# Optimization experiments

Hardware: AMD Instinct MI355X
Metric: run time of the kernel (lower is better)

The kernel has to match this reference:

```python
import jax, jax.numpy as jnp
import numpy as np

KS = (8, 8, 8)   # kernel_size
ST = (4, 4, 4)   # stride


def setup_inputs() -> dict:
    key = jax.random.key(0)
    x = jax.random.normal(key, (1, 16, 8, 8, 8, 4096), dtype=jnp.float32)
    return {"x": x}


def reference(x) -> jnp.ndarray:
    # x: (b, c, k1, k2, k3, l) with l = n**3 windows (n1 slowest, n3 fastest)
    b, c = x.shape[0], x.shape[1]
    l = x.shape[-1]
    n = round(l ** (1.0 / 3.0))
    h = ST[0] * (n - 1) + KS[0]
    w = ST[1] * (n - 1) + KS[1]
    d = ST[2] * (n - 1) + KS[2]

    # (b,c,k1,k2,k3,n1,n2,n3) -> (b,c,n1,k1,n2,k2,n3,k3) -> merge window/patch dims
    xr = x.reshape(b, c, KS[0], KS[1], KS[2], n, n, n)
    xr = xr.transpose(0, 1, 5, 2, 6, 3, 7, 4)
    xr = xr.reshape(b, c, n * KS[0], n * KS[1], n * KS[2])

    def make_idx(k, s):
        # flattened output position for (window, in-window offset) pairs
        return (jnp.arange(n)[:, None] * s + jnp.arange(k)[None, :]).reshape(-1)

    i1 = make_idx(KS[0], ST[0])
    i2 = make_idx(KS[1], ST[1])
    i3 = make_idx(KS[2], ST[2])

    out = jnp.zeros((b, c, h, w, d), dtype=x.dtype)
    out = out.at[:, :, i1[:, None, None], i2[None, :, None], i3[None, None, :]].add(xr)
    return out
```

## Files before the change

kernel.cpp:

```cpp
#include <hip/hip_runtime.h>


#define TOTAL_THREADS (16 * 68 * 68 * 17)

__global__ __launch_bounds__(256) void fold_kernel(const float* __restrict__ x,
                                                   float* __restrict__ out) {
    int t = blockIdx.x * 256 + threadIdx.x;
    int m3 = t % 17;
    int r  = t / 17;
    int o2 = r % 68;
    r /= 68;
    int o1 = r % 68;
    int c  = r / 68;

    int m1 = o1 >> 2, kl1 = o1 & 3;
    int m2 = o2 >> 2, kl2 = o2 & 3;

    float acc0 = 0.f, acc1 = 0.f, acc2 = 0.f, acc3 = 0.f;

#pragma unroll
    for (int kh1 = 0; kh1 < 2; ++kh1) {
        int n1 = m1 - kh1;
        if ((unsigned)n1 >= 16u) continue;
        int k1 = kl1 + 4 * kh1;
#pragma unroll
        for (int kh2 = 0; kh2 < 2; ++kh2) {
            int n2 = m2 - kh2;
            if ((unsigned)n2 >= 16u) continue;
            int k2 = kl2 + 4 * kh2;
            const float* p = x + ((size_t)c << 21) + ((size_t)k1 << 18)
                               + ((size_t)k2 << 15) + (n1 << 8) + (n2 << 4);
#pragma unroll
            for (int kh3 = 0; kh3 < 2; ++kh3) {
                int n3 = m3 - kh3;
                if ((unsigned)n3 >= 16u) continue;
                const float* q = p + ((size_t)(kh3 * 4) << 12) + n3;
                acc0 += q[0 * 4096];
                acc1 += q[1 * 4096];
                acc2 += q[2 * 4096];
                acc3 += q[3 * 4096];
            }
        }
    }

    size_t oidx = ((((size_t)c * 68) + o1) * 68 + o2) * 68 + (m3 << 2);
    float4 v = make_float4(acc0, acc1, acc2, acc3);
    *reinterpret_cast<float4*>(out + oidx) = v;
}

extern "C" void kernel_launch(void* const* d_in, const int* in_sizes, int n_in,
                              void* d_out, int out_size, void* d_ws, size_t ws_size,
                              hipStream_t stream) {
    const float* x = (const float*)d_in[0];
    float* out = (float*)d_out;
    dim3 grid(TOTAL_THREADS / 256), block(256);
    hipLaunchKernelGGL(fold_kernel, grid, block, 0, stream, x, out);
}
```

Before: 197.4 us.

## Remap fold threads to vectorized float4 window loads with lane shuffles for overlap

Each thread now handles one in-window offset kl3 and a block of four consecutive n3 windows. It issues two float4 loads per (kh1, kh2) pair instead of many scalar strided loads. The neighbouring window's overlapping contribution is passed between lanes with shuffles, and the boundary element is written by the b==0 lane. Input reads become vectorized and coalesced, but output stores become scattered scalar stores at stride 4, and the shuffles are placed outside the validity branch so lanes stay uniform.

New measurement: 194.5 us, median of 2. About the same (-1.5%).

```diff
diff --git a/kernel.cpp b/kernel.cpp
--- a/kernel.cpp
+++ b/kernel.cpp
@@ -1,13 +1,14 @@
 #include <hip/hip_runtime.h>
 
 
-#define TOTAL_THREADS (16 * 68 * 68 * 17)
+#define TOTAL_THREADS (16 * 68 * 68 * 16)
 
 __global__ __launch_bounds__(256) void fold_kernel(const float* __restrict__ x,
                                                    float* __restrict__ out) {
     int t = blockIdx.x * 256 + threadIdx.x;
-    int m3 = t % 17;
-    int r  = t / 17;
+    int b   = t & 3;
+    int kl3 = (t >> 2) & 3;
+    int r   = t >> 4;
     int o2 = r % 68;
     r /= 68;
     int o1 = r % 68;
@@ -16,36 +17,48 @@
     int m1 = o1 >> 2, kl1 = o1 & 3;
     int m2 = o2 >> 2, kl2 = o2 & 3;
 
-    float acc0 = 0.f, acc1 = 0.f, acc2 = 0.f, acc3 = 0.f;
+    float a0 = 0.f, a1 = 0.f, a2 = 0.f, a3 = 0.f, a4 = 0.f;
 
 #pragma unroll
     for (int kh1 = 0; kh1 < 2; ++kh1) {
         int n1 = m1 - kh1;
-        if ((unsigned)n1 >= 16u) continue;
+        bool v1 = (unsigned)n1 < 16u;
         int k1 = kl1 + 4 * kh1;
 #pragma unroll
         for (int kh2 = 0; kh2 < 2; ++kh2) {
             int n2 = m2 - kh2;
-            if ((unsigned)n2 >= 16u) continue;
+            bool ok = v1 && ((unsigned)n2 < 16u);
             int k2 = kl2 + 4 * kh2;
-            const float* p = x + ((size_t)c << 21) + ((size_t)k1 << 18)
-                               + ((size_t)k2 << 15) + (n1 << 8) + (n2 << 4);
-#pragma unroll
-            for (int kh3 = 0; kh3 < 2; ++kh3) {
-                int n3 = m3 - kh3;
-                if ((unsigned)n3 >= 16u) continue;
-                const float* q = p + ((size_t)(kh3 * 4) << 12) + n3;
-                acc0 += q[0 * 4096];
-                acc1 += q[1 * 4096];
-                acc2 += q[2 * 4096];
-                acc3 += q[3 * 4096];
+
+            ptrdiff_t base = ((ptrdiff_t)c << 21) + ((ptrdiff_t)k1 << 18)
+                           + ((ptrdiff_t)k2 << 15) + ((ptrdiff_t)n1 << 8)
+                           + ((ptrdiff_t)n2 << 4) + 4 * b;
+
+            float4 A = make_float4(0.f, 0.f, 0.f, 0.f);
+            float4 B = make_float4(0.f, 0.f, 0.f, 0.f);
+            if (ok) {
+                A = *reinterpret_cast<const float4*>(x + base + ((ptrdiff_t)kl3 << 12));
+                B = *reinterpret_cast<const float4*>(x + base + ((ptrdiff_t)(kl3 + 4) << 12));
+            }
+            float s_up = __shfl_up(B.w, 1);
+            float s_dn = __shfl_down(B.w, 3);
+            if (ok) {
+                a0 += A.x;
+                a1 += A.y + B.x;
+                a2 += A.z + B.y;
+                a3 += A.w + B.z;
+                if (b > 0) a0 += s_up;
+                if (b == 0) a4 += s_dn;
             }
         }
     }
 
-    size_t oidx = ((((size_t)c * 68) + o1) * 68 + o2) * 68 + (m3 << 2);
-    float4 v = make_float4(acc0, acc1, acc2, acc3);
-    *reinterpret_cast<float4*>(out + oidx) = v;
+    size_t ob = ((((size_t)c * 68) + o1) * 68 + o2) * 68 + (size_t)(16 * b + kl3);
+    out[ob]      = a0;
+    out[ob + 4]  = a1;
+    out[ob + 8]  = a2;
+    out[ob + 12] = a3;
+    if (b == 0) out[ob + 64] = a4;
 }
 
 extern "C" void kernel_launch(void* const* d_in, const int* in_sizes, int n_in,
```
